# Kernel tuning notes

Hardware: AMD Instinct MI355X
Metric: run time of the kernel (lower is better)

The kernel has to match this reference:

```python
import jax, jax.numpy as jnp
import numpy as np

EPS = 1e-7
T_NCE = 0.07      # opt.nce_t
MOMENTUM = 0.5    # opt.nce_m
N_DATA = 100000   # opt.n_data


def l2norm(x):
    # Normalize(power=2): x / (sum(x^2, dim=1))^(1/2)
    return x / jnp.sqrt(jnp.sum(x * x, axis=1, keepdims=True))


def contrast_loss(x, P):
    # ContrastLoss (Eq 18). x: [B, P+K] of normalized exp-similarities.
    B, PK = x.shape
    N = PK - P
    m_pn = N * (1.0 / N_DATA)  # m * Pn
    pos = x[:, :P]                                   # [B, P]
    log_D1 = jnp.log(pos / (pos + m_pn + EPS))
    neg = x[:, P:]                                   # [B, N]
    log_D0 = jnp.log(m_pn / (neg + m_pn + EPS))
    # log_D0.view(-1,1).repeat(1,P).sum(0) == P copies of log_D0.sum()
    return -((log_D1.sum(0) + log_D0.sum()) / B).sum() / P


def setup_inputs() -> dict:
    key = jax.random.key(0)
    ks = jax.random.split(key, 10)
    B, S_DIM, T_DIM, FEAT = 64, 2048, 2048, 128
    P, K = 4, 8192
    NCLS, PER = 7, 1000
    stdv = 1.0 / np.sqrt(FEAT / 3.0)
    return {
        "f_s": jax.random.normal(ks[0], (B, S_DIM), jnp.float32),
        "f_t": jax.random.normal(ks[1], (B, T_DIM), jnp.float32),
        "idx": jax.random.randint(ks[2], (B,), 0, N_DATA),
        "batch_label": jax.random.uniform(ks[3], (B, NCLS), dtype=jnp.float32),
        "class_index": jax.random.randint(ks[4], (NCLS, PER), 0, N_DATA),
        "num_pos": P,
        "contrast_idx": jax.random.randint(ks[5], (B, P + K), 0, N_DATA),
        "W_s": jax.random.normal(ks[6], (S_DIM, FEAT), jnp.float32) * 0.02,
        "b_s": jnp.zeros((FEAT,), jnp.float32),
        "W_t": jax.random.normal(ks[7], (T_DIM, FEAT), jnp.float32) * 0.02,
        "b_t": jnp.zeros((FEAT,), jnp.float32),
        "memory_s": jax.random.uniform(ks[8], (N_DATA, FEAT), jnp.float32, -stdv, stdv),
        "memory_t": jax.random.uniform(ks[9], (N_DATA, FEAT), jnp.float32, -stdv, stdv),
    }


def reference(f_s, f_t, idx, batch_label, class_index, num_pos, contrast_idx,
              W_s, b_s, W_t, b_t, memory_s, memory_t):
    # Embed + L2 norm
    f_s = l2norm(f_s @ W_s + b_s)   # [B, D]
    f_t = l2norm(f_t @ W_t + b_t)   # [B, D]

    # ContrastMemory (memory banks are buffers -> no grad through them)
    mem_s = jax.lax.stop_gradient(memory_s)
    mem_t = jax.lax.stop_gradient(memory_t)

    w_t = mem_t[contrast_idx]                                     # [B, P+K, D]
    out_s = jnp.exp(jnp.einsum('bkd,bd->bk', w_t, f_s) / T_NCE)
    out_s = out_s / (jnp.mean(out_s) * N_DATA)                    # Z_s normalization
    w_s = mem_s[contrast_idx]                                     # [B, P+K, D]
    out_t = jnp.exp(jnp.einsum('bkd,bd->bk', w_s, f_t) / T_NCE)
    out_t = out_t / (jnp.mean(out_t) * N_DATA)                    # Z_t normalization

    # momentum memory update (done under no_grad in torch)
    upd_s = l2norm(mem_s[idx] * MOMENTUM + jax.lax.stop_gradient(f_s) * (1.0 - MOMENTUM))
    new_mem_s = mem_s.at[idx].set(upd_s)
    upd_t = l2norm(mem_t[idx] * MOMENTUM + jax.lax.stop_gradient(f_t) * (1.0 - MOMENTUM))
    new_mem_t = mem_t.at[idx].set(upd_t)

    CCD_loss = contrast_loss(out_s, num_pos) + contrast_loss(out_t, num_pos)

    # class-center anchors: gather per-class memory rows, relu, mean -> [NCLS, D]
    s_anchors = l2norm(jnp.mean(jax.nn.relu(new_mem_s[class_index]), axis=1))
    t_anchors = l2norm(jnp.mean(jax.nn.relu(new_mem_t[class_index]), axis=1))

    # anchor relation loss (anchors detached; teacher relation fully detached)
    s_rel = (f_s @ jax.lax.stop_gradient(s_anchors).T) / T_NCE    # [B, NCLS]
    t_rel = jax.lax.stop_gradient((f_t @ t_anchors.T) / T_NCE)
    targets = jax.nn.softmax(t_rel, axis=1)
    log_inputs = jax.nn.log_softmax(s_rel, axis=1)
    relation_loss = jnp.sum(targets * (jnp.log(targets + EPS * 0 + 1e-30) - log_inputs)) / s_rel.shape[0]

    return (CCD_loss, relation_loss, f_s, f_t)
```

## Files before the change

kernel.cpp:

```cpp
#include <hip/hip_runtime.h>
#include <math.h>
#include <stdint.h>

#define B 64
#define SDIM 2048
#define FEAT 128
#define P 4
#define PK 8196
#define NCLS 7
#define PER 1000
#define NDATA 100000
#define EPSC 1e-7f
#define M_PN 0.08192f
#define JCHUNKS 50
#define CS (PER / JCHUNKS)

#define DTSZ (64 * NDATA)
#define KSPLIT 4
#define KSEG 2049
#define KS1 8
#define RPB 128

#define TILE 16
#define WCHUNK 512
#define NT (WCHUNK / TILE)

#define GLL16(gp, lp) \
    __builtin_amdgcn_global_load_lds( \
        (__attribute__((address_space(1))) void*)(uintptr_t)(gp), \
        (__attribute__((address_space(3))) void*)(lp), 16, 0, 0)

typedef __attribute__((ext_vector_type(8))) short bf16x8;
typedef __attribute__((ext_vector_type(4))) float f32x4;

static __device__ __forceinline__ short f2bf(float x)
{
    union { float f; uint32_t u; } v; v.f = x;
    const uint32_t r = (v.u + 0x7fffu + ((v.u >> 16) & 1u)) >> 16;
    return (short)r;
}

__global__ void gemm_partial_kernel(const float* __restrict__ f_s,
                                    const float* __restrict__ f_t,
                                    const float* __restrict__ W_s,
                                    const float* __restrict__ W_t,
                                    float* __restrict__ fb)
{
    const int row = blockIdx.x;
    const int z   = blockIdx.y;
    const int ks  = blockIdx.z;
    const float* f = z == 0 ? f_s : f_t;
    const float* W = z == 0 ? W_s : W_t;

    const int t  = threadIdx.x;
    const int d  = t & 127;
    const int kh = t >> 7;

    __shared__ float frow[SDIM / KS1];
    frow[t] = f[row * SDIM + ks * (SDIM / KS1) + t];
    __syncthreads();

    float acc = 0.0f;
    const int kb = ks * (SDIM / KS1) + kh * 128;
    #pragma unroll 8
    for (int k = 0; k < 128; ++k)
        acc = fmaf(frow[kh * 128 + k], W[(kb + k) * FEAT + d], acc);

    __shared__ float part[2][128];
    part[kh][d] = acc;
    __syncthreads();
    if (t < 128)
        atomicAdd(&fb[((size_t)z * B + row) * FEAT + t], part[0][t] + part[1][t]);
}

__global__ void norm_finish_kernel(const float* __restrict__ fb,
                                   const float* __restrict__ b_s,
                                   const float* __restrict__ b_t,
                                   float* __restrict__ out_fs,
                                   float* __restrict__ out_ft,
                                   float* __restrict__ fsw,
                                   float* __restrict__ ftw,
                                   unsigned short* __restrict__ fsb,
                                   unsigned short* __restrict__ ftb)
{
    const int row = blockIdx.x;
    const int z   = blockIdx.y;
    const int d   = threadIdx.x;
    const float* bias = z == 0 ? b_s : b_t;
    float* out = z == 0 ? out_fs : out_ft;
    float* fw  = z == 0 ? fsw : ftw;
    unsigned short* fbx = z == 0 ? fsb : ftb;

    const float a = fb[((size_t)z * B + row) * FEAT + d] + bias[d];
    __shared__ float red[128];
    red[d] = a * a;
    __syncthreads();
    for (int s = 64; s > 0; s >>= 1) {
        if (d < s) red[d] += red[d + s];
        __syncthreads();
    }
    const float v = a * (1.0f / sqrtf(red[0]));
    out[row * FEAT + d] = v;
    fw[row * FEAT + d]  = v;
    fbx[row * FEAT + d] = (unsigned short)f2bf(v);
}

#define DECL_AB(p) float4 p##lo0, p##hi0, p##lo1, p##hi1, \
                          p##lo2, p##hi2, p##lo3, p##hi3
#define LOAD_AB(p, ap) do { \
    p##lo0 = *(const float4*)((ap) +  0); p##hi0 = *(const float4*)((ap) +  4); \
    p##lo1 = *(const float4*)((ap) + 32); p##hi1 = *(const float4*)((ap) + 36); \
    p##lo2 = *(const float4*)((ap) + 64); p##hi2 = *(const float4*)((ap) + 68); \
    p##lo3 = *(const float4*)((ap) + 96); p##hi3 = *(const float4*)((ap) + 100); \
    } while (0)
#define CVT8(lo, hi) (bf16x8){ f2bf((lo).x), f2bf((lo).y), f2bf((lo).z), f2bf((lo).w), \
                               f2bf((hi).x), f2bf((hi).y), f2bf((hi).z), f2bf((hi).w) }
#define MFMA4(av, kc, a0, a1, a2, a3) do { \
    a0 = __builtin_amdgcn_mfma_f32_16x16x32_bf16(av, bv[kc][0], a0, 0, 0, 0); \
    a1 = __builtin_amdgcn_mfma_f32_16x16x32_bf16(av, bv[kc][1], a1, 0, 0, 0); \
    a2 = __builtin_amdgcn_mfma_f32_16x16x32_bf16(av, bv[kc][2], a2, 0, 0, 0); \
    a3 = __builtin_amdgcn_mfma_f32_16x16x32_bf16(av, bv[kc][3], a3, 0, 0, 0); \
    } while (0)

__global__ __launch_bounds__(256, 2)
void dgemm3_kernel(const unsigned short* __restrict__ fsb,
                   const unsigned short* __restrict__ ftb,
                   const float* __restrict__ mem_s,
                   const float* __restrict__ mem_t,
                   float* __restrict__ DT0,
                   float* __restrict__ DT1,
                   int zbase)
{
    const int z = blockIdx.y + zbase;
    const unsigned short* fWb = z == 0 ? fsb : ftb;
    const float* mem          = z == 0 ? mem_t : mem_s;
    float* DT                 = z == 0 ? DT0 : DT1;

    const int tid = threadIdx.x;
    const int w   = tid >> 6;
    const int l   = tid & 63;
    const int ln  = l & 15;
    const int ko  = l >> 4;
    const int rbase = blockIdx.x * RPB + w * 32;

    int ar0 = rbase + ln;        if (ar0 >= NDATA) ar0 = NDATA - 1;
    int ar1 = rbase + 16 + ln;   if (ar1 >= NDATA) ar1 = NDATA - 1;
    const float* ap0 = mem + (size_t)ar0 * FEAT + ko * 8;
    const float* ap1 = mem + (size_t)ar1 * FEAT + ko * 8;
    DECL_AB(Aa);
    DECL_AB(Ab);
    LOAD_AB(Aa, ap0);
    LOAD_AB(Ab, ap1);

    bf16x8 bv[4][4];
    #pragma unroll
    for (int kc = 0; kc < 4; ++kc)
        #pragma unroll
        for (int nt = 0; nt < 4; ++nt)
            bv[kc][nt] = *(const bf16x8*)(fWb + (nt * 16 + ln) * FEAT + kc * 32 + ko * 8);

    __builtin_amdgcn_sched_barrier(0);

    {
        f32x4 c0 = (f32x4){0.f,0.f,0.f,0.f};
        f32x4 c1 = (f32x4){0.f,0.f,0.f,0.f};
        f32x4 c2 = (f32x4){0.f,0.f,0.f,0.f};
        f32x4 c3 = (f32x4){0.f,0.f,0.f,0.f};
        { const bf16x8 av = CVT8(Aalo0, Aahi0); MFMA4(av, 0, c0, c1, c2, c3); }
        { const bf16x8 av = CVT8(Aalo1, Aahi1); MFMA4(av, 1, c0, c1, c2, c3); }
        { const bf16x8 av = CVT8(Aalo2, Aahi2); MFMA4(av, 2, c0, c1, c2, c3); }
        { const bf16x8 av = CVT8(Aalo3, Aahi3); MFMA4(av, 3, c0, c1, c2, c3); }
        const int grow = rbase + ko * 4;
        if (grow < NDATA) {
            *(f32x4*)(DT + (size_t)( 0 + ln) * NDATA + grow) = c0;
            *(f32x4*)(DT + (size_t)(16 + ln) * NDATA + grow) = c1;
            *(f32x4*)(DT + (size_t)(32 + ln) * NDATA + grow) = c2;
            *(f32x4*)(DT + (size_t)(48 + ln) * NDATA + grow) = c3;
        }
    }
    {
        f32x4 c0 = (f32x4){0.f,0.f,0.f,0.f};
        f32x4 c1 = (f32x4){0.f,0.f,0.f,0.f};
        f32x4 c2 = (f32x4){0.f,0.f,0.f,0.f};
        f32x4 c3 = (f32x4){0.f,0.f,0.f,0.f};
        { const bf16x8 av = CVT8(Ablo0, Abhi0); MFMA4(av, 0, c0, c1, c2, c3); }
        { const bf16x8 av = CVT8(Ablo1, Abhi1); MFMA4(av, 1, c0, c1, c2, c3); }
        { const bf16x8 av = CVT8(Ablo2, Abhi2); MFMA4(av, 2, c0, c1, c2, c3); }
        { const bf16x8 av = CVT8(Ablo3, Abhi3); MFMA4(av, 3, c0, c1, c2, c3); }
        const int grow = rbase + 16 + ko * 4;
        if (grow < NDATA) {
            *(f32x4*)(DT + (size_t)( 0 + ln) * NDATA + grow) = c0;
            *(f32x4*)(DT + (size_t)(16 + ln) * NDATA + grow) = c1;
            *(f32x4*)(DT + (size_t)(32 + ln) * NDATA + grow) = c2;
            *(f32x4*)(DT + (size_t)(48 + ln) * NDATA + grow) = c3;
        }
    }
}

__global__ void gather2_kernel(const int* __restrict__ contrast_idx,
                               const float* __restrict__ DT0,
                               const float* __restrict__ DT1,
                               float* __restrict__ out_raw,
                               float* __restrict__ Ssum)
{
    const int z   = blockIdx.z;
    const int b   = blockIdx.y;
    const int ks  = blockIdx.x;
    const int tid = threadIdx.x;
    const int k0  = ks * KSEG;
    const int kend = min(k0 + KSEG, PK);
    const float inv_t = 1.0f / 0.07f;
    const float* dtb = (z == 0 ? DT0 : DT1) + (size_t)b * NDATA;
    float* orz = out_raw + (size_t)z * (B * PK);
    float lsum = 0.0f;
    #pragma unroll 4
    for (int k = k0 + tid; k < kend; k += 256) {
        const int ci = contrast_idx[(size_t)b * PK + k];
        const float v = expf(dtb[ci] * inv_t);
        orz[(size_t)b * PK + k] = v;
        lsum += v;
    }
    __shared__ float red[256];
    red[tid] = lsum;
    __syncthreads();
    for (int s = 128; s > 0; s >>= 1) {
        if (tid < s) red[tid] += red[tid + s];
        __syncthreads();
    }
    if (tid == 0) atomicAdd(&Ssum[z], red[0]);
}

__global__ void gemm_norm_kernel(const float* __restrict__ f_s,
                                 const float* __restrict__ f_t,
                                 const float* __restrict__ W_s,
                                 const float* __restrict__ b_s,
                                 const float* __restrict__ W_t,
                                 const float* __restrict__ b_t,
                                 float* __restrict__ out_fs,
                                 float* __restrict__ out_ft)
{
    const int row = blockIdx.x;
    const int z   = blockIdx.y;
    const float* f    = z == 0 ? f_s : f_t;
    const float* W    = z == 0 ? W_s : W_t;
    const float* bias = z == 0 ? b_s : b_t;
    float* out        = z == 0 ? out_fs : out_ft;

    __shared__ __align__(16) float frow[SDIM];
    const int t  = threadIdx.x;
    const int d  = t & 127;
    const int kh = t >> 7;
    for (int k = t; k < SDIM; k += 256) frow[k] = f[row * SDIM + k];
    __syncthreads();

    float acc = 0.0f;
    const int k0 = kh * (SDIM / 2);
    for (int k = k0; k < k0 + SDIM / 2; ++k)
        acc = fmaf(frow[k], W[k * FEAT + d], acc);

    __shared__ float part[2][128];
    part[kh][d] = acc;
    __syncthreads();
    const float a = part[0][d] + part[1][d] + bias[d];

    __shared__ float red[256];
    red[t] = (t < 128) ? a * a : 0.0f;
    __syncthreads();
    for (int s = 128; s > 0; s >>= 1) {
        if (t < s) red[t] += red[t + s];
        __syncthreads();
    }
    if (t < 128) out[row * FEAT + t] = a * (1.0f / sqrtf(red[0]));
}

__global__ __launch_bounds__(64)
void dots_kernel(const float* __restrict__ fsn,
                 const float* __restrict__ ftn,
                 const int*   __restrict__ contrast_idx,
                 const float* __restrict__ mem_s,
                 const float* __restrict__ mem_t,
                 float* __restrict__ out_raw,
                 float* __restrict__ Ssum)
{
    const int z = blockIdx.z;
    const int b = blockIdx.y;
    const int l = threadIdx.x;
    const int kchunk = blockIdx.x * WCHUNK;

    const float* f   = (z == 0 ? fsn : ftn) + b * FEAT;
    const float* mem = (z == 0 ? mem_t : mem_s);

    __shared__ __align__(16) float rows[2][TILE * FEAT];
    __shared__ __align__(16) float fl[FEAT];
    __shared__ int cis[WCHUNK];

    fl[l]      = f[l];
    fl[l + 64] = f[l + 64];
    for (int i = l; i < WCHUNK; i += 64) {
        const int k = kchunk + i;
        cis[i] = contrast_idx[(size_t)b * PK + (k < PK ? k : PK - 1)];
    }
    __syncthreads();

    const int q   = l >> 4;
    const int r_c = l & 15;
    const int xk  = r_c & 7;
    const int rh  = l >> 5;
    const int sl  = l & 31;

    const float4* fg = (const float4*)fl;
    const float4 f0 = fg[q * 8 + 0], f1 = fg[q * 8 + 1];
    const float4 f2 = fg[q * 8 + 2], f3 = fg[q * 8 + 3];
    const float4 f4 = fg[q * 8 + 4], f5 = fg[q * 8 + 5];
    const float4 f6 = fg[q * 8 + 6], f7 = fg[q * 8 + 7];

    const float inv_t = 1.0f / 0.07f;
    const size_t obase = (size_t)z * (B * PK) + (size_t)b * PK;
    float lsum = 0.0f;

#define STAGE(tt, bf) do { \
    _Pragma("unroll") \
    for (int p_ = 0; p_ < 8; ++p_) { \
        const int rr_ = 2 * p_ + rh; \
        const int ci_ = cis[(tt) * TILE + rr_]; \
        const float* g_ = mem + (size_t)ci_ * FEAT + ((sl ^ (rr_ & 7)) << 2); \
        GLL16(g_, &rows[bf][p_ * 256]); \
    } } while (0)

    STAGE(0, 0);
    int cur = 0;
    for (int t = 0; t < NT; ++t) {
        if (t + 1 < NT) {
            STAGE(t + 1, cur ^ 1);
            asm volatile("s_waitcnt vmcnt(8)" ::: "memory");
        } else {
            asm volatile("s_waitcnt vmcnt(0)" ::: "memory");
        }
        __builtin_amdgcn_sched_barrier(0);

        const float* rbase = &rows[cur][r_c * FEAT];
        float dot;
        {
            const float4 m0 = *(const float4*)(rbase + (((q * 8 + 0) ^ xk) << 2));
            const float4 m1 = *(const float4*)(rbase + (((q * 8 + 1) ^ xk) << 2));
            const float4 m2 = *(const float4*)(rbase + (((q * 8 + 2) ^ xk) << 2));
            const float4 m3 = *(const float4*)(rbase + (((q * 8 + 3) ^ xk) << 2));
            const float4 m4 = *(const float4*)(rbase + (((q * 8 + 4) ^ xk) << 2));
            const float4 m5 = *(const float4*)(rbase + (((q * 8 + 5) ^ xk) << 2));
            const float4 m6 = *(const float4*)(rbase + (((q * 8 + 6) ^ xk) << 2));
            const float4 m7 = *(const float4*)(rbase + (((q * 8 + 7) ^ xk) << 2));
            dot = m0.x * f0.x;
            dot = fmaf(m0.y, f0.y, dot); dot = fmaf(m0.z, f0.z, dot); dot = fmaf(m0.w, f0.w, dot);
            dot = fmaf(m1.x, f1.x, dot); dot = fmaf(m1.y, f1.y, dot); dot = fmaf(m1.z, f1.z, dot); dot = fmaf(m1.w, f1.w, dot);
            dot = fmaf(m2.x, f2.x, dot); dot = fmaf(m2.y, f2.y, dot); dot = fmaf(m2.z, f2.z, dot); dot = fmaf(m2.w, f2.w, dot);
            dot = fmaf(m3.x, f3.x, dot); dot = fmaf(m3.y, f3.y, dot); dot = fmaf(m3.z, f3.z, dot); dot = fmaf(m3.w, f3.w, dot);
            dot = fmaf(m4.x, f4.x, dot); dot = fmaf(m4.y, f4.y, dot); dot = fmaf(m4.z, f4.z, dot); dot = fmaf(m4.w, f4.w, dot);
            dot = fmaf(m5.x, f5.x, dot); dot = fmaf(m5.y, f5.y, dot); dot = fmaf(m5.z, f5.z, dot); dot = fmaf(m5.w, f5.w, dot);
            dot = fmaf(m6.x, f6.x, dot); dot = fmaf(m6.y, f6.y, dot); dot = fmaf(m6.z, f6.z, dot); dot = fmaf(m6.w, f6.w, dot);
            dot = fmaf(m7.x, f7.x, dot); dot = fmaf(m7.y, f7.y, dot); dot = fmaf(m7.z, f7.z, dot); dot = fmaf(m7.w, f7.w, dot);
        }
        dot += __shfl_xor(dot, 16);
        dot += __shfl_xor(dot, 32);

        const int krow = kchunk + t * TILE + r_c;
        if (q == 0 && krow < PK) {
            const float val = expf(dot * inv_t);
            out_raw[obase + krow] = val;
            lsum += val;
        }
        cur ^= 1;
    }
#undef STAGE

    lsum += __shfl_xor(lsum, 8);
    lsum += __shfl_xor(lsum, 4);
    lsum += __shfl_xor(lsum, 2);
    lsum += __shfl_xor(lsum, 1);
    if (l == 0) atomicAdd(&Ssum[z], lsum);
}

__global__ void ccd_loss_kernel(const float* __restrict__ out_raw,
                                const float* __restrict__ Ssum,
                                float* __restrict__ acc)
{
    const int z = blockIdx.y;
    const float S = Ssum[z];
    const float c = ((float)(B * PK)) / (S * (float)NDATA);

    const int total = B * PK;
    float contrib = 0.0f;
    for (int i = blockIdx.x * blockDim.x + threadIdx.x; i < total;
         i += gridDim.x * blockDim.x) {
        const float v = out_raw[(size_t)z * total + i] * c;
        const int k = i % PK;
        if (k < P) {
            contrib += logf(v / (v + M_PN + EPSC));
        } else {
            contrib += (float)P * logf(M_PN / (v + M_PN + EPSC));
        }
    }
    __shared__ float red[256];
    red[threadIdx.x] = contrib;
    __syncthreads();
    for (int s = 128; s > 0; s >>= 1) {
        if (threadIdx.x < s) red[threadIdx.x] += red[threadIdx.x + s];
        __syncthreads();
    }
    if (threadIdx.x == 0) atomicAdd(&acc[z], red[0]);
}

__global__ void upd_kernel(const float* __restrict__ fsn,
                           const float* __restrict__ ftn,
                           const int*   __restrict__ idx,
                           const float* __restrict__ mem_s,
                           const float* __restrict__ mem_t,
                           float* __restrict__ upd)
{
    const int z = blockIdx.y;
    const int b = blockIdx.x;
    const int d = threadIdx.x;
    const float* mem = z == 0 ? mem_s : mem_t;
    const float* f   = z == 0 ? fsn : ftn;
    const int i = idx[b];
    const float v = mem[(size_t)i * FEAT + d] * 0.5f + f[b * FEAT + d] * 0.5f;
    __shared__ float red[128];
    red[d] = v * v;
    __syncthreads();
    for (int s = 64; s > 0; s >>= 1) {
        if (d < s) red[d] += red[d + s];
        __syncthreads();
    }
    upd[(size_t)z * (B * FEAT) + b * FEAT + d] = v * (1.0f / sqrtf(red[0]));
}

__global__ void remap_kernel(const int* __restrict__ class_index,
                             const int* __restrict__ idx,
                             int* __restrict__ remap)
{
    const int e = blockIdx.x * 256 + threadIdx.x;
    if (e >= NCLS * PER) return;
    const int ci = class_index[e];
    int rb = -1;
    for (int b = B - 1; b >= 0; --b) {
        if (idx[b] == ci) { rb = b; break; }
    }
    remap[e] = rb;
}

__global__ void anchors_partial_kernel(const int* __restrict__ class_index,
                                       const int* __restrict__ remap,
                                       const float* __restrict__ mem_s,
                                       const float* __restrict__ mem_t,
                                       const float* __restrict__ upd,
                                       float* __restrict__ partial)
{
    const int z     = blockIdx.z;
    const int c     = blockIdx.y;
    const int chunk = blockIdx.x;
    const int d     = threadIdx.x;
    const float* mem = z == 0 ? mem_s : mem_t;
    const float* u   = upd + (size_t)z * (B * FEAT);
    float acc = 0.0f;
    #pragma unroll 4
    for (int j = chunk * CS; j < chunk * CS + CS; ++j) {
        const int e = c * PER + j;
        const int ci = class_index[e];
        const int rb = remap[e];
        const float* row = (rb >= 0) ? (u + rb * FEAT) : (mem + (size_t)ci * FEAT);
        const float v = row[d];
        acc += v > 0.0f ? v : 0.0f;
    }
    atomicAdd(&partial[(size_t)z * (NCLS * FEAT) + c * FEAT + d], acc);
}

__global__ void anchors_finish_kernel(const float* __restrict__ partial,
                                      float* __restrict__ anchors)
{
    const int z = blockIdx.y;
    const int c = blockIdx.x;
    const int d = threadIdx.x;
    const float meanv = partial[(size_t)z * (NCLS * FEAT) + c * FEAT + d]
                        * (1.0f / (float)PER);
    __shared__ float red[128];
    red[d] = meanv * meanv;
    __syncthreads();
    for (int s = 64; s > 0; s >>= 1) {
        if (d < s) red[d] += red[d + s];
        __syncthreads();
    }
    anchors[(size_t)z * (NCLS * FEAT) + c * FEAT + d] = meanv * (1.0f / sqrtf(red[0]));
}

__global__ void final_kernel(const float* __restrict__ fsn,
                             const float* __restrict__ ftn,
                             const float* __restrict__ anchors,
                             const float* __restrict__ acc,
                             float* __restrict__ d_out)
{
    __shared__ float sa[NCLS * FEAT];
    __shared__ float ta[NCLS * FEAT];
    const int tid = threadIdx.x;
    for (int i = tid; i < NCLS * FEAT; i += 64) {
        sa[i] = anchors[i];
        ta[i] = anchors[NCLS * FEAT + i];
    }
    __syncthreads();

    const int b = tid;
    float srel[NCLS], trel[NCLS];
    for (int j = 0; j < NCLS; ++j) { srel[j] = 0.0f; trel[j] = 0.0f; }
    for (int d = 0; d < FEAT; ++d) {
        const float fs = fsn[b * FEAT + d];
        const float ft = ftn[b * FEAT + d];
        #pragma unroll
        for (int j = 0; j < NCLS; ++j) {
            srel[j] = fmaf(fs, sa[j * FEAT + d], srel[j]);
            trel[j] = fmaf(ft, ta[j * FEAT + d], trel[j]);
        }
    }
    const float inv_t = 1.0f / 0.07f;
    float smax = -1e30f, tmax = -1e30f;
    for (int j = 0; j < NCLS; ++j) {
        srel[j] *= inv_t; trel[j] *= inv_t;
        smax = fmaxf(smax, srel[j]);
        tmax = fmaxf(tmax, trel[j]);
    }
    float ssum = 0.0f, tsum = 0.0f;
    float texp[NCLS];
    for (int j = 0; j < NCLS; ++j) {
        ssum += expf(srel[j] - smax);
        texp[j] = expf(trel[j] - tmax);
        tsum += texp[j];
    }
    const float lse_s = logf(ssum);
    float contrib = 0.0f;
    for (int j = 0; j < NCLS; ++j) {
        const float tgt = texp[j] / tsum;
        const float log_in = srel[j] - smax - lse_s;
        contrib += tgt * (logf(tgt + 1e-30f) - log_in);
    }
    for (int off = 32; off > 0; off >>= 1) contrib += __shfl_down(contrib, off);
    if (tid == 0) {
        d_out[1] = contrib / (float)B;
        d_out[0] = -(acc[0] + acc[1]) / (float)(B * P);
    }
}

extern "C" void kernel_launch(void* const* d_in, const int* in_sizes, int n_in,
                              void* d_out_v, int out_size, void* d_ws, size_t ws_size,
                              hipStream_t stream)
{
    const float* f_s = (const float*)d_in[0];
    const float* f_t = (const float*)d_in[1];
    const int*   idx = (const int*)d_in[2];
    const int*   class_index = (const int*)d_in[4];
    const int*   contrast_idx = (const int*)d_in[6];
    const float* W_s = (const float*)d_in[7];
    const float* b_s = (const float*)d_in[8];
    const float* W_t = (const float*)d_in[9];
    const float* b_t = (const float*)d_in[10];
    const float* mem_s = (const float*)d_in[11];
    const float* mem_t = (const float*)d_in[12];

    float* out    = (float*)d_out_v;
    float* out_fs = out + 2;
    float* out_ft = out + 2 + B * FEAT;

    float* ws = (float*)d_ws;
    const size_t fl = ws_size / sizeof(float);
    const size_t REST = 2 * (size_t)B * PK
                      + 2 * B * FEAT
                      + 2 * (B * FEAT / 2)
                      + 2 * B * FEAT
                      + 2 * B * FEAT
                      + 4 * NCLS * FEAT
                      + NCLS * PER
                      + 64;
    const bool big   = fl >= 2 * (size_t)DTSZ + REST;
    const bool small = fl >= 1 * (size_t)DTSZ + REST;

    if (small) {
        float* DT0 = ws;
        float* DT1 = big ? ws + DTSZ : DT0;
        float* p   = (big ? ws + 2 * (size_t)DTSZ : ws + DTSZ);
        float* out_raw = p;            p += 2 * (size_t)B * PK;
        float* fsw     = p;            p += B * FEAT;
        float* ftw     = p;            p += B * FEAT;
        unsigned short* fsb = (unsigned short*)p;  p += B * FEAT / 2;
        unsigned short* ftb = (unsigned short*)p;  p += B * FEAT / 2;
        float* fb      = p;            p += 2 * B * FEAT;
        float* partial = p;            p += 2 * NCLS * FEAT;
        float* Ssum    = p;            p += 2;
        float* acc     = p;            p += 2;
        float* upd     = p;            p += 2 * B * FEAT;
        float* anchors = p;            p += 2 * NCLS * FEAT;
        int*   remap   = (int*)p;

        hipMemsetAsync(fb, 0,
                       (2 * B * FEAT + 2 * NCLS * FEAT + 4) * sizeof(float),
                       stream);

        dim3 g1a(B, 2, KS1);
        gemm_partial_kernel<<<g1a, 256, 0, stream>>>(f_s, f_t, W_s, W_t, fb);
        dim3 g1b(B, 2);
        norm_finish_kernel<<<g1b, 128, 0, stream>>>(fb, b_s, b_t,
                                                    out_fs, out_ft,
                                                    fsw, ftw, fsb, ftb);

        const int gblocks = (NDATA + RPB - 1) / RPB;
        if (big) {
            dim3 gd(gblocks, 2);
            dgemm3_kernel<<<gd, 256, 0, stream>>>(fsb, ftb, mem_s, mem_t,
                                                  DT0, DT1, 0);
            dim3 gg(KSPLIT, B, 2);
            gather2_kernel<<<gg, 256, 0, stream>>>(contrast_idx, DT0, DT1,
                                                   out_raw, Ssum);
        } else {
            dim3 gd(gblocks, 1);
            dim3 gg(KSPLIT, B, 1);
            dgemm3_kernel<<<gd, 256, 0, stream>>>(fsb, ftb, mem_s, mem_t,
                                                  DT0, DT0, 0);
            gather2_kernel<<<gg, 256, 0, stream>>>(contrast_idx, DT0, DT0,
                                                   out_raw, Ssum);
            dgemm3_kernel<<<gd, 256, 0, stream>>>(fsb, ftb, mem_s, mem_t,
                                                  DT0, DT0, 1);
            gather2_kernel<<<gg, 256, 0, stream>>>(contrast_idx, DT0, DT0,
                                                   out_raw + (size_t)B * PK,
                                                   Ssum + 1);
        }

        dim3 g3(256, 2);
        ccd_loss_kernel<<<g3, 256, 0, stream>>>(out_raw, Ssum, acc);
        dim3 g4(B, 2);
        upd_kernel<<<g4, 128, 0, stream>>>(out_fs, out_ft, idx, mem_s, mem_t, upd);
        remap_kernel<<<(NCLS * PER + 255) / 256, 256, 0, stream>>>(class_index, idx, remap);
        dim3 g5a(JCHUNKS, NCLS, 2);
        anchors_partial_kernel<<<g5a, 128, 0, stream>>>(class_index, remap,
                                                        mem_s, mem_t, upd, partial);
        dim3 g5b(NCLS, 2);
        anchors_finish_kernel<<<g5b, 128, 0, stream>>>(partial, anchors);
        final_kernel<<<1, 64, 0, stream>>>(out_fs, out_ft, anchors, acc, out);
    } else {
        float* out_raw = ws;
        float* upd     = out_raw + 2 * (B * PK);
        float* anchors = upd + 2 * (B * FEAT);
        float* partial = anchors + 2 * (NCLS * FEAT);
        float* Ssum    = partial + 2 * (NCLS * FEAT);
        float* acc     = Ssum + 2;
        int*   remap   = (int*)(acc + 2);

        hipMemsetAsync(partial, 0, (2 * NCLS * FEAT + 4) * sizeof(float), stream);

        dim3 g1(B, 2);
        gemm_norm_kernel<<<g1, 256, 0, stream>>>(f_s, f_t, W_s, b_s, W_t, b_t,
                                                 out_fs, out_ft);
        dim3 g2((PK + WCHUNK - 1) / WCHUNK, B, 2);
        dots_kernel<<<g2, 64, 0, stream>>>(out_fs, out_ft, contrast_idx,
                                           mem_s, mem_t, out_raw, Ssum);
        dim3 g3(256, 2);
        ccd_loss_kernel<<<g3, 256, 0, stream>>>(out_raw, Ssum, acc);
        dim3 g4(B, 2);
        upd_kernel<<<g4, 128, 0, stream>>>(out_fs, out_ft, idx, mem_s, mem_t, upd);
        remap_kernel<<<(NCLS * PER + 255) / 256, 256, 0, stream>>>(class_index, idx, remap);
        dim3 g5a(JCHUNKS, NCLS, 2);
        anchors_partial_kernel<<<g5a, 128, 0, stream>>>(class_index, remap,
                                                        mem_s, mem_t, upd, partial);
        dim3 g5b(NCLS, 2);
        anchors_finish_kernel<<<g5b, 128, 0, stream>>>(partial, anchors);
        final_kernel<<<1, 64, 0, stream>>>(out_fs, out_ft, anchors, acc, out);
    }
}
```

Before: 120.3 us.

## Stream memory-bank rows through double-buffered LDS with direct global-to-LDS loads

The dense memory-bank GEMM kernel now gives each wave 4 tiles of 16 rows instead of 2, and it double-buffers them in LDS through global_load_lds with an XOR swizzle. The next tile's load overlaps the MFMAs on the current tile, controlled by explicit vmcnt waits. This is meant to hide global-load latency and cut register pressure from holding raw fp32 rows in VGPRs. In exchange it uses 64KB of LDS per block, which may limit occupancy, and it halves the grid size.

```diff
diff --git a/kernel.cpp b/kernel.cpp
--- a/kernel.cpp
+++ b/kernel.cpp
@@ -19,7 +19,8 @@
 #define KSPLIT 4
 #define KSEG 2049
 #define KS1 8
-#define RPB 128
+#define TPW 4
+#define ROWS_BLK (4 * TPW * 16)
 
 #define TILE 16
 #define WCHUNK 512
@@ -105,16 +106,6 @@
     fbx[row * FEAT + d] = (unsigned short)f2bf(v);
 }
 
-#define DECL_AB(p) float4 p##lo0, p##hi0, p##lo1, p##hi1, \
-                          p##lo2, p##hi2, p##lo3, p##hi3
-#define LOAD_AB(p, ap) do { \
-    p##lo0 = *(const float4*)((ap) +  0); p##hi0 = *(const float4*)((ap) +  4); \
-    p##lo1 = *(const float4*)((ap) + 32); p##hi1 = *(const float4*)((ap) + 36); \
-    p##lo2 = *(const float4*)((ap) + 64); p##hi2 = *(const float4*)((ap) + 68); \
-    p##lo3 = *(const float4*)((ap) + 96); p##hi3 = *(const float4*)((ap) + 100); \
-    } while (0)
-#define CVT8(lo, hi) (bf16x8){ f2bf((lo).x), f2bf((lo).y), f2bf((lo).z), f2bf((lo).w), \
-                               f2bf((hi).x), f2bf((hi).y), f2bf((hi).z), f2bf((hi).w) }
 #define MFMA4(av, kc, a0, a1, a2, a3) do { \
     a0 = __builtin_amdgcn_mfma_f32_16x16x32_bf16(av, bv[kc][0], a0, 0, 0, 0); \
     a1 = __builtin_amdgcn_mfma_f32_16x16x32_bf16(av, bv[kc][1], a1, 0, 0, 0); \
@@ -123,7 +114,7 @@
     } while (0)
 
 __global__ __launch_bounds__(256, 2)
-void dgemm3_kernel(const unsigned short* __restrict__ fsb,
+void dgemm4_kernel(const unsigned short* __restrict__ fsb,
                    const unsigned short* __restrict__ ftb,
                    const float* __restrict__ mem_s,
                    const float* __restrict__ mem_t,
@@ -141,16 +132,10 @@
     const int l   = tid & 63;
     const int ln  = l & 15;
     const int ko  = l >> 4;
-    const int rbase = blockIdx.x * RPB + w * 32;
-
-    int ar0 = rbase + ln;        if (ar0 >= NDATA) ar0 = NDATA - 1;
-    int ar1 = rbase + 16 + ln;   if (ar1 >= NDATA) ar1 = NDATA - 1;
-    const float* ap0 = mem + (size_t)ar0 * FEAT + ko * 8;
-    const float* ap1 = mem + (size_t)ar1 * FEAT + ko * 8;
-    DECL_AB(Aa);
-    DECL_AB(Ab);
-    LOAD_AB(Aa, ap0);
-    LOAD_AB(Ab, ap1);
+    const int xk  = ln & 7;
+    const int wrowbase = blockIdx.x * ROWS_BLK + w * (TPW * 16);
+
+    __shared__ __align__(16) float rows[4][2][16 * FEAT];
 
     bf16x8 bv[4][4];
     #pragma unroll
@@ -159,42 +144,52 @@
         for (int nt = 0; nt < 4; ++nt)
             bv[kc][nt] = *(const bf16x8*)(fWb + (nt * 16 + ln) * FEAT + kc * 32 + ko * 8);
 
-    __builtin_amdgcn_sched_barrier(0);
-
-    {
+#define STG(tt, bf) do { \
+    _Pragma("unroll") \
+    for (int p_ = 0; p_ < 8; ++p_) { \
+        const int r_ = 2 * p_ + (l >> 5); \
+        int gr_ = wrowbase + (tt) * 16 + r_; \
+        if (gr_ >= NDATA) gr_ = NDATA - 1; \
+        const float* g_ = mem + (size_t)gr_ * FEAT + (((l & 31) ^ (r_ & 7)) << 2); \
+        GLL16(g_, &rows[w][bf][p_ * 256]); \
+    } } while (0)
+
+    STG(0, 0);
+    int cur = 0;
+    for (int t = 0; t < TPW; ++t) {
+        if (t + 1 < TPW) {
+            STG(t + 1, cur ^ 1);
+            asm volatile("s_waitcnt vmcnt(8)" ::: "memory");
+        } else {
+            asm volatile("s_waitcnt vmcnt(0)" ::: "memory");
+        }
+        __builtin_amdgcn_sched_barrier(0);
+
+        const float* rb = &rows[w][cur][ln * FEAT];
         f32x4 c0 = (f32x4){0.f,0.f,0.f,0.f};
         f32x4 c1 = (f32x4){0.f,0.f,0.f,0.f};
         f32x4 c2 = (f32x4){0.f,0.f,0.f,0.f};
         f32x4 c3 = (f32x4){0.f,0.f,0.f,0.f};
-        { const bf16x8 av = CVT8(Aalo0, Aahi0); MFMA4(av, 0, c0, c1, c2, c3); }
-        { const bf16x8 av = CVT8(Aalo1, Aahi1); MFMA4(av, 1, c0, c1, c2, c3); }
-        { const bf16x8 av = CVT8(Aalo2, Aahi2); MFMA4(av, 2, c0, c1, c2, c3); }
-        { const bf16x8 av = CVT8(Aalo3, Aahi3); MFMA4(av, 3, c0, c1, c2, c3); }
-        const int grow = rbase + ko * 4;
-        if (grow < NDATA) {
-            *(f32x4*)(DT + (size_t)( 0 + ln) * NDATA + grow) = c0;
-            *(f32x4*)(DT + (size_t)(16 + ln) * NDATA + grow) = c1;
-            *(f32x4*)(DT + (size_t)(32 + ln) * NDATA + grow) = c2;
-            *(f32x4*)(DT + (size_t)(48 + ln) * NDATA + grow) = c3;
-        }
-    }
-    {
-        f32x4 c0 = (f32x4){0.f,0.f,0.f,0.f};
-        f32x4 c1 = (f32x4){0.f,0.f,0.f,0.f};
-        f32x4 c2 = (f32x4){0.f,0.f,0.f,0.f};
-        f32x4 c3 = (f32x4){0.f,0.f,0.f,0.f};
-        { const bf16x8 av = CVT8(Ablo0, Abhi0); MFMA4(av, 0, c0, c1, c2, c3); }
-        { const bf16x8 av = CVT8(Ablo1, Abhi1); MFMA4(av, 1, c0, c1, c2, c3); }
-        { const bf16x8 av = CVT8(Ablo2, Abhi2); MFMA4(av, 2, c0, c1, c2, c3); }
-        { const bf16x8 av = CVT8(Ablo3, Abhi3); MFMA4(av, 3, c0, c1, c2, c3); }
-        const int grow = rbase + 16 + ko * 4;
-        if (grow < NDATA) {
-            *(f32x4*)(DT + (size_t)( 0 + ln) * NDATA + grow) = c0;
-            *(f32x4*)(DT + (size_t)(16 + ln) * NDATA + grow) = c1;
-            *(f32x4*)(DT + (size_t)(32 + ln) * NDATA + grow) = c2;
-            *(f32x4*)(DT + (size_t)(48 + ln) * NDATA + grow) = c3;
-        }
-    }
+        #pragma unroll
+        for (int kc = 0; kc < 4; ++kc) {
+            const int g0 = kc * 8 + ko * 2;
+            const float4 lo = *(const float4*)(rb + (((g0 + 0) ^ xk) << 2));
+            const float4 hi = *(const float4*)(rb + (((g0 + 1) ^ xk) << 2));
+            const bf16x8 av = (bf16x8){ f2bf(lo.x), f2bf(lo.y), f2bf(lo.z), f2bf(lo.w),
+                                        f2bf(hi.x), f2bf(hi.y), f2bf(hi.z), f2bf(hi.w) };
+            MFMA4(av, kc, c0, c1, c2, c3);
+        }
+
+        const int growb = wrowbase + t * 16 + ko * 4;
+        if (growb < NDATA) {
+            *(f32x4*)(DT + (size_t)( 0 + ln) * NDATA + growb) = c0;
+            *(f32x4*)(DT + (size_t)(16 + ln) * NDATA + growb) = c1;
+            *(f32x4*)(DT + (size_t)(32 + ln) * NDATA + growb) = c2;
+            *(f32x4*)(DT + (size_t)(48 + ln) * NDATA + growb) = c3;
+        }
+        cur ^= 1;
+    }
+#undef STG
 }
 
 __global__ void gather2_kernel(const int* __restrict__ contrast_idx,
@@ -607,10 +602,10 @@
                                                     out_fs, out_ft,
                                                     fsw, ftw, fsb, ftb);
 
-        const int gblocks = (NDATA + RPB - 1) / RPB;
+        const int gblocks = (NDATA + ROWS_BLK - 1) / ROWS_BLK;
         if (big) {
             dim3 gd(gblocks, 2);
-            dgemm3_kernel<<<gd, 256, 0, stream>>>(fsb, ftb, mem_s, mem_t,
+            dgemm4_kernel<<<gd, 256, 0, stream>>>(fsb, ftb, mem_s, mem_t,
                                                   DT0, DT1, 0);
             dim3 gg(KSPLIT, B, 2);
             gather2_kernel<<<gg, 256, 0, stream>>>(contrast_idx, DT0, DT1,
@@ -618,11 +613,11 @@
         } else {
             dim3 gd(gblocks, 1);
             dim3 gg(KSPLIT, B, 1);
-            dgemm3_kernel<<<gd, 256, 0, stream>>>(fsb, ftb, mem_s, mem_t,
+            dgemm4_kernel<<<gd, 256, 0, stream>>>(fsb, ftb, mem_s, mem_t,
                                                   DT0, DT0, 0);
             gather2_kernel<<<gg, 256, 0, stream>>>(contrast_idx, DT0, DT0,
                                                    out_raw, Ssum);
-            dgemm3_kernel<<<gd, 256, 0, stream>>>(fsb, ftb, mem_s, mem_t,
+            dgemm4_kernel<<<gd, 256, 0, stream>>>(fsb, ftb, mem_s, mem_t,
                                                   DT0, DT0, 1);
             gather2_kernel<<<gg, 256, 0, stream>>>(contrast_idx, DT0, DT0,
                                                    out_raw + (size_t)B * PK,
```

New measurement: 118.6 us. About the same (-1.4%).
